# Kernel tuning notes

Hardware: AMD Instinct MI355X
Metric: run time of the kernel (lower is better)

The kernel has to match this reference:

```python
import jax, jax.numpy as jnp
import numpy as np

EPSILON = 0.0014  # ODIN perturbation magnitude (init kwarg)


def _penultimate(x, W, b):
    # Simple feature extractor standing in for model.penultimate_forward:
    # flatten image and apply ReLU(linear). feat: [B, D]
    B = x.shape[0]
    return jax.nn.relu(x.reshape(B, -1) @ W + b)


def _mahalanobis_scores(feat, mu, invsig):
    # diff: [B, C, D]; y[b,c] = -diff[b,c] @ invsig @ diff[b,c]
    # Fused as a single einsum instead of the naive [B,C,D,D] broadcast.
    diff = feat[:, None, :] - mu[None, :, :]
    return -jnp.einsum('bcd,de,bce->bc', diff, invsig, diff)


def setup_inputs() -> dict:
    key = jax.random.key(0)
    k1, k2, k3, k4, k5 = jax.random.split(key, 5)
    B, C, D, IN = 1024, 100, 512, 3 * 32 * 32
    x = jax.random.uniform(k1, (B, 3, 32, 32), dtype=jnp.float32)
    W = jax.random.normal(k2, (IN, D), dtype=jnp.float32) * (1.0 / np.sqrt(IN))
    b = jax.random.normal(k3, (D,), dtype=jnp.float32) * 0.01
    mu = jax.random.normal(k4, (C, D), dtype=jnp.float32)
    # symmetric positive-definite inverse covariance
    A = jax.random.normal(k5, (D, D), dtype=jnp.float32) * (1.0 / np.sqrt(D))
    invsig = A @ A.T + jnp.eye(D, dtype=jnp.float32)
    return {"x": x, "W": W, "b": b, "mu": mu, "invsig": invsig}


def reference(x, W, b, mu, invsig):
    # FGSM step: perturb x toward increasing the max class score.
    def fgsm_loss(xx):
        y = _mahalanobis_scores(_penultimate(xx, W, b), mu, invsig)
        return jnp.max(y, axis=1).sum()

    g = jax.grad(fgsm_loss)(x)
    # torch.autograd.grad(create_graph=False) detaches the grad -> stop_gradient
    x_adv = jnp.clip(x + EPSILON * jax.lax.stop_gradient(g), 0.0, 1.0)
    # Main pass on the perturbed input.
    return _mahalanobis_scores(_penultimate(x_adv, W, b), mu, invsig)
```

## Files before the change

### kernel.cpp

```cpp
#include <hip/hip_runtime.h>
#include <hip/hip_bf16.h>

#define EPS_ODIN 0.0014f

constexpr int Bb  = 1024;
constexpr int Cc  = 100;
constexpr int Dd  = 512;
constexpr int INn = 3072;
constexpr int PITCH = 68;

using s16x8 = __attribute__((ext_vector_type(8))) short;
using s16x4 = __attribute__((ext_vector_type(4))) short;
using f32x4 = __attribute__((ext_vector_type(4))) float;

__device__ __forceinline__ short f2bf(float f) {
    __hip_bfloat16 h = __float2bfloat16(f);
    return *reinterpret_cast<short*>(&h);
}

__global__ __launch_bounds__(256) void prep_kernel(
    const float* __restrict__ x, const float* __restrict__ W,
    const float* __restrict__ invsig, const float* __restrict__ mu,
    short* __restrict__ x_b, short* __restrict__ Wt_b,
    short* __restrict__ is_b, short* __restrict__ mu_b)
{
    __shared__ float tp[32][33];
    const int tid = threadIdx.x, bid = blockIdx.x;
    const long gstride = (long)gridDim.x * 256;
    auto cvt4 = [&](const float* in, short* ob, long q) {
        long idx = q * 4;
        f32x4 v = *(const f32x4*)(in + idx);
        s16x4 o;
        #pragma unroll
        for (int j = 0; j < 4; ++j) o[j] = f2bf(v[j]);
        *(s16x4*)(ob + idx) = o;
    };
    for (long i = (long)bid * 256 + tid; i < (long)Bb * INn / 4; i += gstride) cvt4(x, x_b, i);
    for (long i = (long)bid * 256 + tid; i < (long)Dd * Dd / 4; i += gstride) cvt4(invsig, is_b, i);
    for (long i = (long)bid * 256 + tid; i < (long)112 * Dd / 4; i += gstride) {
        long idx = i * 4;
        if ((idx >> 9) < Cc) cvt4(mu, mu_b, i);
        else *(s16x4*)(mu_b + idx) = s16x4{0, 0, 0, 0};
    }

    const int tx = tid & 31, ty = tid >> 5;
    for (int tix = bid; tix < (INn / 32) * (Dd / 32); tix += gridDim.x) {
        int r0 = (tix >> 4) * 32, c0 = (tix & 15) * 32;
        #pragma unroll
        for (int i2 = 0; i2 < 4; ++i2)
            tp[ty + i2 * 8][tx] = W[(long)(r0 + ty + i2 * 8) * Dd + c0 + tx];
        __syncthreads();
        #pragma unroll
        for (int i2 = 0; i2 < 4; ++i2) {
            int c = c0 + ty + i2 * 8;
            Wt_b[(long)c * INn + r0 + tx] = f2bf(tp[tx][ty + i2 * 8]);
        }
        __syncthreads();
    }
}

__global__ __launch_bounds__(256) void im_q_kernel(
    const float* __restrict__ mu, const float* __restrict__ invsig,
    float* __restrict__ im, float* __restrict__ q)
{
    __shared__ float muc[512];
    __shared__ float red[4];
    const int tid = threadIdx.x, c = blockIdx.x;
    for (int e = tid; e < 512; e += 256) muc[e] = mu[(long)c * 512 + e];
    __syncthreads();
    const int d0 = tid, d1 = tid + 256;
    float a0 = 0.f, a1 = 0.f, a2 = 0.f, a3 = 0.f;
    for (int e = 0; e < 512; e += 2) {
        float m0 = muc[e], m1 = muc[e + 1];
        a0 = fmaf(m0, invsig[(long)e * 512 + d0], a0);
        a1 = fmaf(m0, invsig[(long)e * 512 + d1], a1);
        a2 = fmaf(m1, invsig[(long)(e + 1) * 512 + d0], a2);
        a3 = fmaf(m1, invsig[(long)(e + 1) * 512 + d1], a3);
    }
    float r0 = a0 + a2, r1 = a1 + a3;
    im[(long)c * 512 + d0] = r0;
    im[(long)c * 512 + d1] = r1;
    float s = muc[d0] * r0 + muc[d1] * r1;
    #pragma unroll
    for (int off = 32; off; off >>= 1) s += __shfl_down(s, off);
    if ((tid & 63) == 0) red[tid >> 6] = s;
    __syncthreads();
    if (tid == 0) q[c] = red[0] + red[1] + red[2] + red[3];
}

template<int EPI>
__global__ __launch_bounds__(256, 4) void gemm_b1(
    const short* __restrict__ A, const short* __restrict__ Bm,
    float* __restrict__ Cm, long K, int kcount, int N, long sstr,
    const float* __restrict__ aux1, const float* __restrict__ aux2,
    short* __restrict__ obf, float esc)
{
    __shared__ short As[128 * PITCH];
    __shared__ short Bs[64 * PITCH];
    const int tid = threadIdx.x;
    const int m0 = blockIdx.y * 128, n0 = blockIdx.x * 64;
    const long kbeg = (long)blockIdx.z * kcount;
    const int lane = tid & 63, w = tid >> 6, wm = w * 32;
    const int lrow = lane & 15, kseg = lane >> 4;
    const int srow = tid >> 3, skc = (tid & 7) * 8;
    const int nkt = kcount >> 6;

    f32x4 acc[2][4];
    #pragma unroll
    for (int i = 0; i < 2; ++i)
        #pragma unroll
        for (int j = 0; j < 4; ++j)
            acc[i][j] = f32x4{0.f, 0.f, 0.f, 0.f};

    s16x8 rA[4], rB[2];
    auto ldA = [&](int kt) {
        #pragma unroll
        for (int i = 0; i < 4; ++i)
            rA[i] = *(const s16x8*)(A + (long)(m0 + srow + i * 32) * K + kbeg + (long)kt * 64 + skc);
    };
    auto ldB = [&](int kt) {
        #pragma unroll
        for (int i = 0; i < 2; ++i)
            rB[i] = *(const s16x8*)(Bm + (long)(n0 + srow + i * 32) * K + kbeg + (long)kt * 64 + skc);
    };

    ldA(0); ldB(0);
    for (int kt = 0; kt < nkt; ++kt) {
        #pragma unroll
        for (int i = 0; i < 4; ++i)
            *(s16x8*)&As[(srow + i * 32) * PITCH + skc] = rA[i];
        #pragma unroll
        for (int i = 0; i < 2; ++i)
            *(s16x8*)&Bs[(srow + i * 32) * PITCH + skc] = rB[i];
        __syncthreads();
        if (kt + 1 < nkt) { ldA(kt + 1); ldB(kt + 1); }
        #pragma unroll
        for (int kk = 0; kk < 2; ++kk) {
            s16x8 ah[2], bfr[4];
            #pragma unroll
            for (int i = 0; i < 2; ++i)
                ah[i] = *(const s16x8*)&As[(wm + i * 16 + lrow) * PITCH + kk * 32 + kseg * 8];
            #pragma unroll
            for (int j = 0; j < 4; ++j)
                bfr[j] = *(const s16x8*)&Bs[(j * 16 + lrow) * PITCH + kk * 32 + kseg * 8];
            #pragma unroll
            for (int i = 0; i < 2; ++i)
                #pragma unroll
                for (int j = 0; j < 4; ++j)
                    acc[i][j] = __builtin_amdgcn_mfma_f32_16x16x32_bf16(ah[i], bfr[j], acc[i][j], 0, 0, 0);
        }
        __syncthreads();
    }

    const int crow = (lane >> 4) * 4, ccol = lane & 15;
    #pragma unroll
    for (int i = 0; i < 2; ++i)
        #pragma unroll
        for (int j = 0; j < 4; ++j)
            #pragma unroll
            for (int r = 0; r < 4; ++r) {
                int gm = m0 + wm + i * 16 + crow + r;
                int gn = n0 + j * 16 + ccol;
                float v = acc[i][j][r];
                if (EPI == 0) {
                    (Cm + (long)blockIdx.z * sstr)[(long)gm * 512 + gn] = v;
                } else if (EPI == 1) {
                    long cidx = (long)gm * N + gn;
                    Cm[cidx] = v;
                    obf[cidx] = f2bf(v);
                } else {
                    long cidx = (long)gm * N + gn;
                    float u = fmaxf(aux1[cidx] + aux2[gn] + esc * v, 0.f);
                    Cm[cidx] = u;
                    obf[cidx] = f2bf(u);
                }
            }
}

__global__ __launch_bounds__(256) void reduce_feat(
    const float* __restrict__ part, const float* __restrict__ bias,
    float* __restrict__ featpre, float* __restrict__ feat, short* __restrict__ fb)
{
    long idx = ((long)blockIdx.x * 256 + threadIdx.x) * 4;
    f32x4 v = *(const f32x4*)(part + idx);
    #pragma unroll
    for (int z = 1; z < 4; ++z)
        v += *(const f32x4*)(part + (long)z * Bb * Dd + idx);
    *(f32x4*)(featpre + idx) = v;
    f32x4 bb = *(const f32x4*)(bias + (idx & 511));
    s16x4 o;
    #pragma unroll
    for (int j = 0; j < 4; ++j) {
        v[j] = fmaxf(v[j] + bb[j], 0.f);
        o[j] = f2bf(v[j]);
    }
    *(f32x4*)(feat + idx) = v;
    *(s16x4*)(fb + idx) = o;
}

__global__ __launch_bounds__(256) void reduce_wtw(
    const float* __restrict__ wpart, short* __restrict__ wtw_b)
{
    long idx = ((long)blockIdx.x * 256 + threadIdx.x) * 4;
    f32x4 v = *(const f32x4*)(wpart + idx);
    #pragma unroll
    for (int z = 1; z < 4; ++z)
        v += *(const f32x4*)(wpart + (long)z * Dd * Dd + idx);
    s16x4 o;
    #pragma unroll
    for (int j = 0; j < 4; ++j) o[j] = f2bf(v[j]);
    *(s16x4*)(wtw_b + idx) = o;
}

__global__ __launch_bounds__(256) void tail_a(
    const short* __restrict__ h_b, const short* __restrict__ mu_b,
    const float* __restrict__ feat, const float* __restrict__ hbuf,
    const float* __restrict__ im, const float* __restrict__ q,
    short* __restrict__ dz_b)
{
    __shared__ f32x4 red[4][7][64];
    __shared__ int cstv[16];
    const int tid = threadIdx.x, lane = tid & 63, w = tid >> 6;
    const int m0 = blockIdx.x * 16;
    const int arow = lane & 15, kseg = lane >> 4;

    f32x4 acc[7];
    #pragma unroll
    for (int j = 0; j < 7; ++j) acc[j] = f32x4{0.f, 0.f, 0.f, 0.f};

    const long abase = (long)(m0 + arow) * 512 + w * 128 + kseg * 8;
    const long bbase = (long)arow * 512 + w * 128 + kseg * 8;
    #pragma unroll
    for (int kt = 0; kt < 4; ++kt) {
        s16x8 av = *(const s16x8*)(h_b + abase + kt * 32);
        #pragma unroll
        for (int j = 0; j < 7; ++j) {
            s16x8 bv = *(const s16x8*)(mu_b + bbase + (long)j * 16 * 512 + kt * 32);
            acc[j] = __builtin_amdgcn_mfma_f32_16x16x32_bf16(av, bv, acc[j], 0, 0, 0);
        }
    }
    #pragma unroll
    for (int j = 0; j < 7; ++j) red[w][j][lane] = acc[j];
    __syncthreads();

    if (w == 0) {
        #pragma unroll
        for (int j = 0; j < 7; ++j) {
            f32x4 s0 = red[0][j][lane];
            #pragma unroll
            for (int ww = 1; ww < 4; ++ww) s0 += red[ww][j][lane];
            acc[j] = s0;
        }
        const int crow = (lane >> 4) * 4, ccol = lane & 15;
        #pragma unroll
        for (int r = 0; r < 4; ++r) {
            float best = -INFINITY; int bestc = 0;
            #pragma unroll
            for (int j = 0; j < 7; ++j) {
                int n = j * 16 + ccol;
                if (n < 100) {
                    float v = 2.f * acc[j][r] - q[n];
                    if (v > best) { best = v; bestc = n; }
                }
            }
            #pragma unroll
            for (int mk = 1; mk <= 8; mk <<= 1) {
                float ov = __shfl_xor(best, mk);
                int   oc = __shfl_xor(bestc, mk);
                if (ov > best || (ov == best && oc < bestc)) { best = ov; bestc = oc; }
            }
            if (ccol == 0) cstv[crow + r] = bestc;
        }
    }
    __syncthreads();

    #pragma unroll
    for (int it = 0; it < 8; ++it) {
        int i4 = it * 256 + tid;
        int r = i4 >> 7, d4 = (i4 & 127) * 4;
        long gi = (long)(m0 + r) * 512 + d4;
        f32x4 fv = *(const f32x4*)(feat + gi);
        f32x4 hv = *(const f32x4*)(hbuf + gi);
        f32x4 iv = *(const f32x4*)(im + (long)cstv[r] * 512 + d4);
        s16x4 o;
        #pragma unroll
        for (int jj = 0; jj < 4; ++jj) {
            float v = (fv[jj] > 0.f) ? -2.f * (hv[jj] - iv[jj]) : 0.f;
            o[jj] = f2bf(v);
        }
        *(s16x4*)(dz_b + gi) = o;
    }
}

__global__ __launch_bounds__(256) void tail_b(
    const short* __restrict__ h_b, const short* __restrict__ mu_b,
    const float* __restrict__ feat, const float* __restrict__ hbuf,
    const float* __restrict__ q, float* __restrict__ out)
{
    __shared__ f32x4 red[4][7][64];
    __shared__ float srow[16];
    const int tid = threadIdx.x, lane = tid & 63, w = tid >> 6;
    const int m0 = blockIdx.x * 16;
    const int arow = lane & 15, kseg = lane >> 4;

    #pragma unroll
    for (int rr = 0; rr < 4; ++rr) {
        int r = w * 4 + rr;
        long gi = (long)(m0 + r) * 512 + lane * 8;
        f32x4 a0 = *(const f32x4*)(feat + gi);
        f32x4 a1 = *(const f32x4*)(feat + gi + 4);
        f32x4 b0 = *(const f32x4*)(hbuf + gi);
        f32x4 b1 = *(const f32x4*)(hbuf + gi + 4);
        float ss = 0.f;
        #pragma unroll
        for (int jj = 0; jj < 4; ++jj) ss += a0[jj] * b0[jj] + a1[jj] * b1[jj];
        #pragma unroll
        for (int off = 32; off; off >>= 1) ss += __shfl_down(ss, off);
        if (lane == 0) srow[r] = ss;
    }

    f32x4 acc[7];
    #pragma unroll
    for (int j = 0; j < 7; ++j) acc[j] = f32x4{0.f, 0.f, 0.f, 0.f};
    const long abase = (long)(m0 + arow) * 512 + w * 128 + kseg * 8;
    const long bbase = (long)arow * 512 + w * 128 + kseg * 8;
    #pragma unroll
    for (int kt = 0; kt < 4; ++kt) {
        s16x8 av = *(const s16x8*)(h_b + abase + kt * 32);
        #pragma unroll
        for (int j = 0; j < 7; ++j) {
            s16x8 bv = *(const s16x8*)(mu_b + bbase + (long)j * 16 * 512 + kt * 32);
            acc[j] = __builtin_amdgcn_mfma_f32_16x16x32_bf16(av, bv, acc[j], 0, 0, 0);
        }
    }
    #pragma unroll
    for (int j = 0; j < 7; ++j) red[w][j][lane] = acc[j];
    __syncthreads();

    if (w == 0) {
        const int crow = (lane >> 4) * 4, ccol = lane & 15;
        #pragma unroll
        for (int j = 0; j < 7; ++j) {
            int n = j * 16 + ccol;
            if (n >= 100) continue;
            f32x4 s0 = red[0][j][lane];
            #pragma unroll
            for (int ww = 1; ww < 4; ++ww) s0 += red[ww][j][lane];
            float qn = q[n];
            #pragma unroll
            for (int r = 0; r < 4; ++r)
                out[(long)(m0 + crow + r) * 100 + n] = 2.f * s0[r] - srow[crow + r] - qn;
        }
    }
}

extern "C" void kernel_launch(void* const* d_in, const int* in_sizes, int n_in,
                              void* d_out, int out_size, void* d_ws, size_t ws_size,
                              hipStream_t stream)
{
    const float* x      = (const float*)d_in[0];
    const float* W      = (const float*)d_in[1];
    const float* bias   = (const float*)d_in[2];
    const float* mu     = (const float*)d_in[3];
    const float* invsig = (const float*)d_in[4];
    float* out = (float*)d_out;

    char* wp = (char*)d_ws;
    auto alloc = [&](size_t bytes) { char* p = wp; wp += (bytes + 255) & ~size_t(255); return p; };
    short* x_b   = (short*)alloc((size_t)Bb * INn * 2);
    short* Wt_b  = (short*)alloc((size_t)Dd * INn * 2);
    short* is_b  = (short*)alloc((size_t)Dd * Dd * 2);
    short* mu_b  = (short*)alloc((size_t)112 * Dd * 2);
    short* wtw_b = (short*)alloc((size_t)Dd * Dd * 2);
    float* im    = (float*)alloc((size_t)Cc * Dd * 4);
    float* q     = (float*)alloc(512);
    float* part  = (float*)alloc((size_t)4 * Bb * Dd * 4);
    float* wpart = (float*)alloc((size_t)4 * Dd * Dd * 4);
    float* featpre = (float*)alloc((size_t)Bb * Dd * 4);
    float* feat  = (float*)alloc((size_t)Bb * Dd * 4);
    short* f_b   = (short*)alloc((size_t)Bb * Dd * 2);
    float* hbuf  = (float*)alloc((size_t)Bb * Dd * 4);
    short* h_b   = (short*)alloc((size_t)Bb * Dd * 2);
    short* dz_b  = (short*)alloc((size_t)Bb * Dd * 2);

    dim3 blk(256);

    prep_kernel<<<512, blk, 0, stream>>>(x, W, invsig, mu, x_b, Wt_b, is_b, mu_b);
    im_q_kernel<<<Cc, blk, 0, stream>>>(mu, invsig, im, q);
    gemm_b1<0><<<dim3(8, 4, 4), blk, 0, stream>>>(
        Wt_b, Wt_b, wpart, INn, INn / 4, Dd, (long)Dd * Dd, nullptr, nullptr, nullptr, 0.f);
    reduce_wtw<<<256, blk, 0, stream>>>(wpart, wtw_b);
    gemm_b1<0><<<dim3(8, 8, 4), blk, 0, stream>>>(
        x_b, Wt_b, part, INn, INn / 4, Dd, (long)Bb * Dd, nullptr, nullptr, nullptr, 0.f);
    reduce_feat<<<512, blk, 0, stream>>>(part, bias, featpre, feat, f_b);
    gemm_b1<1><<<dim3(8, 8), blk, 0, stream>>>(
        f_b, is_b, hbuf, Dd, Dd, Dd, 0, nullptr, nullptr, h_b, 0.f);
    tail_a<<<Bb / 16, blk, 0, stream>>>(h_b, mu_b, feat, hbuf, im, q, dz_b);
    gemm_b1<3><<<dim3(8, 8), blk, 0, stream>>>(
        dz_b, wtw_b, feat, Dd, Dd, Dd, 0, featpre, bias, f_b, EPS_ODIN);
    gemm_b1<1><<<dim3(8, 8), blk, 0, stream>>>(
        f_b, is_b, hbuf, Dd, Dd, Dd, 0, nullptr, nullptr, h_b, 0.f);
    tail_b<<<Bb / 16, blk, 0, stream>>>(h_b, mu_b, feat, hbuf, q, out);
}
```

Baseline: 109.2 us.

## Fold mu·invsig rows into invsig GEMM to compute class scores directly

Appends the precomputed rows invsig·mu_c (in bf16) under invsig, so a single GEMM of features against this 640-row matrix yields both h = f·invsig and f·invsig·mu_c. The tail kernels then no longer run a second MFMA product of h against mu, and they shrink to 4 rows per block with simple argmax and score assembly. This removes the bf16 rounding of h before the class dot product and the h_b buffer, at the cost of an extra column tile in the GEMM and a different rounding path (mu folded through invsig in fp32 and then rounded).

Result: faster. 99.99 us (median of 2 runs) (-8.5%).

```diff
diff --git a/kernel.cpp b/kernel.cpp
--- a/kernel.cpp
+++ b/kernel.cpp
@@ -20,9 +20,8 @@
 
 __global__ __launch_bounds__(256) void prep_kernel(
     const float* __restrict__ x, const float* __restrict__ W,
-    const float* __restrict__ invsig, const float* __restrict__ mu,
-    short* __restrict__ x_b, short* __restrict__ Wt_b,
-    short* __restrict__ is_b, short* __restrict__ mu_b)
+    const float* __restrict__ invsig,
+    short* __restrict__ x_b, short* __restrict__ Wt_b, short* __restrict__ ism_b)
 {
     __shared__ float tp[32][33];
     const int tid = threadIdx.x, bid = blockIdx.x;
@@ -36,12 +35,9 @@
         *(s16x4*)(ob + idx) = o;
     };
     for (long i = (long)bid * 256 + tid; i < (long)Bb * INn / 4; i += gstride) cvt4(x, x_b, i);
-    for (long i = (long)bid * 256 + tid; i < (long)Dd * Dd / 4; i += gstride) cvt4(invsig, is_b, i);
-    for (long i = (long)bid * 256 + tid; i < (long)112 * Dd / 4; i += gstride) {
-        long idx = i * 4;
-        if ((idx >> 9) < Cc) cvt4(mu, mu_b, i);
-        else *(s16x4*)(mu_b + idx) = s16x4{0, 0, 0, 0};
-    }
+    for (long i = (long)bid * 256 + tid; i < (long)Dd * Dd / 4; i += gstride) cvt4(invsig, ism_b, i);
+    for (long i = (long)bid * 256 + tid; i < 28 * 512 / 4; i += gstride)
+        *(s16x4*)(ism_b + (long)612 * 512 + i * 4) = s16x4{0, 0, 0, 0};
 
     const int tx = tid & 31, ty = tid >> 5;
     for (int tix = bid; tix < (INn / 32) * (Dd / 32); tix += gridDim.x) {
@@ -61,7 +57,7 @@
 
 __global__ __launch_bounds__(256) void im_q_kernel(
     const float* __restrict__ mu, const float* __restrict__ invsig,
-    float* __restrict__ im, float* __restrict__ q)
+    float* __restrict__ im, float* __restrict__ q, short* __restrict__ ism_b)
 {
     __shared__ float muc[512];
     __shared__ float red[4];
@@ -80,6 +76,8 @@
     float r0 = a0 + a2, r1 = a1 + a3;
     im[(long)c * 512 + d0] = r0;
     im[(long)c * 512 + d1] = r1;
+    ism_b[(long)(512 + c) * 512 + d0] = f2bf(r0);
+    ism_b[(long)(512 + c) * 512 + d1] = f2bf(r1);
     float s = muc[d0] * r0 + muc[d1] * r1;
     #pragma unroll
     for (int off = 32; off; off >>= 1) s += __shfl_down(s, off);
@@ -164,10 +162,6 @@
                 float v = acc[i][j][r];
                 if (EPI == 0) {
                     (Cm + (long)blockIdx.z * sstr)[(long)gm * 512 + gn] = v;
-                } else if (EPI == 1) {
-                    long cidx = (long)gm * N + gn;
-                    Cm[cidx] = v;
-                    obf[cidx] = f2bf(v);
                 } else {
                     long cidx = (long)gm * N + gn;
                     float u = fmaxf(aux1[cidx] + aux2[gn] + esc * v, 0.f);
@@ -177,6 +171,85 @@
             }
 }
 
+__global__ __launch_bounds__(256, 4) void gemm_ht(
+    const short* __restrict__ A, const short* __restrict__ Bm,
+    float* __restrict__ hbuf, float* __restrict__ tbuf)
+{
+    __shared__ short As[128 * PITCH];
+    __shared__ short Bs[64 * PITCH];
+    const int tid = threadIdx.x;
+    const int m0 = blockIdx.y * 128, n0 = blockIdx.x * 64;
+    const int lane = tid & 63, w = tid >> 6, wm = w * 32;
+    const int lrow = lane & 15, kseg = lane >> 4;
+    const int srow = tid >> 3, skc = (tid & 7) * 8;
+
+    f32x4 acc[2][4];
+    #pragma unroll
+    for (int i = 0; i < 2; ++i)
+        #pragma unroll
+        for (int j = 0; j < 4; ++j)
+            acc[i][j] = f32x4{0.f, 0.f, 0.f, 0.f};
+
+    s16x8 rA[4], rB[2];
+    auto ldA = [&](int kt) {
+        #pragma unroll
+        for (int i = 0; i < 4; ++i)
+            rA[i] = *(const s16x8*)(A + (long)(m0 + srow + i * 32) * 512 + kt * 64 + skc);
+    };
+    auto ldB = [&](int kt) {
+        #pragma unroll
+        for (int i = 0; i < 2; ++i)
+            rB[i] = *(const s16x8*)(Bm + (long)(n0 + srow + i * 32) * 512 + kt * 64 + skc);
+    };
+
+    ldA(0); ldB(0);
+    for (int kt = 0; kt < 8; ++kt) {
+        #pragma unroll
+        for (int i = 0; i < 4; ++i)
+            *(s16x8*)&As[(srow + i * 32) * PITCH + skc] = rA[i];
+        #pragma unroll
+        for (int i = 0; i < 2; ++i)
+            *(s16x8*)&Bs[(srow + i * 32) * PITCH + skc] = rB[i];
+        __syncthreads();
+        if (kt + 1 < 8) { ldA(kt + 1); ldB(kt + 1); }
+        #pragma unroll
+        for (int kk = 0; kk < 2; ++kk) {
+            s16x8 ah[2], bfr[4];
+            #pragma unroll
+            for (int i = 0; i < 2; ++i)
+                ah[i] = *(const s16x8*)&As[(wm + i * 16 + lrow) * PITCH + kk * 32 + kseg * 8];
+            #pragma unroll
+            for (int j = 0; j < 4; ++j)
+                bfr[j] = *(const s16x8*)&Bs[(j * 16 + lrow) * PITCH + kk * 32 + kseg * 8];
+            #pragma unroll
+            for (int i = 0; i < 2; ++i)
+                #pragma unroll
+                for (int j = 0; j < 4; ++j)
+                    acc[i][j] = __builtin_amdgcn_mfma_f32_16x16x32_bf16(ah[i], bfr[j], acc[i][j], 0, 0, 0);
+        }
+        __syncthreads();
+    }
+
+    const int crow = (lane >> 4) * 4, ccol = lane & 15;
+    if (n0 < 512) {
+        #pragma unroll
+        for (int i = 0; i < 2; ++i)
+            #pragma unroll
+            for (int j = 0; j < 4; ++j)
+                #pragma unroll
+                for (int r = 0; r < 4; ++r)
+                    hbuf[(long)(m0 + wm + i * 16 + crow + r) * 512 + n0 + j * 16 + ccol] = acc[i][j][r];
+    } else {
+        #pragma unroll
+        for (int i = 0; i < 2; ++i)
+            #pragma unroll
+            for (int j = 0; j < 4; ++j)
+                #pragma unroll
+                for (int r = 0; r < 4; ++r)
+                    tbuf[(long)(m0 + wm + i * 16 + crow + r) * 128 + (n0 - 512) + j * 16 + ccol] = acc[i][j][r];
+    }
+}
+
 __global__ __launch_bounds__(256) void reduce_feat(
     const float* __restrict__ part, const float* __restrict__ bias,
     float* __restrict__ featpre, float* __restrict__ feat, short* __restrict__ fb)
@@ -212,70 +285,35 @@
     *(s16x4*)(wtw_b + idx) = o;
 }
 
-__global__ __launch_bounds__(256) void tail_a(
-    const short* __restrict__ h_b, const short* __restrict__ mu_b,
+__global__ __launch_bounds__(256) void tail_a2(
+    const float* __restrict__ tbuf, const float* __restrict__ q,
     const float* __restrict__ feat, const float* __restrict__ hbuf,
-    const float* __restrict__ im, const float* __restrict__ q,
-    short* __restrict__ dz_b)
-{
-    __shared__ f32x4 red[4][7][64];
-    __shared__ int cstv[16];
+    const float* __restrict__ im, short* __restrict__ dz_b)
+{
+    __shared__ int cstv[4];
     const int tid = threadIdx.x, lane = tid & 63, w = tid >> 6;
-    const int m0 = blockIdx.x * 16;
-    const int arow = lane & 15, kseg = lane >> 4;
-
-    f32x4 acc[7];
-    #pragma unroll
-    for (int j = 0; j < 7; ++j) acc[j] = f32x4{0.f, 0.f, 0.f, 0.f};
-
-    const long abase = (long)(m0 + arow) * 512 + w * 128 + kseg * 8;
-    const long bbase = (long)arow * 512 + w * 128 + kseg * 8;
-    #pragma unroll
-    for (int kt = 0; kt < 4; ++kt) {
-        s16x8 av = *(const s16x8*)(h_b + abase + kt * 32);
-        #pragma unroll
-        for (int j = 0; j < 7; ++j) {
-            s16x8 bv = *(const s16x8*)(mu_b + bbase + (long)j * 16 * 512 + kt * 32);
-            acc[j] = __builtin_amdgcn_mfma_f32_16x16x32_bf16(av, bv, acc[j], 0, 0, 0);
-        }
-    }
-    #pragma unroll
-    for (int j = 0; j < 7; ++j) red[w][j][lane] = acc[j];
+    const int m0 = blockIdx.x * 4;
+
+    {
+        const float* tr = tbuf + (long)(m0 + w) * 128;
+        float best = 2.f * tr[lane] - q[lane];
+        int bestc = lane;
+        if (lane + 64 < 100) {
+            float v1 = 2.f * tr[lane + 64] - q[lane + 64];
+            if (v1 > best) { best = v1; bestc = lane + 64; }
+        }
+        #pragma unroll
+        for (int mk = 1; mk <= 32; mk <<= 1) {
+            float ov = __shfl_xor(best, mk);
+            int   oc = __shfl_xor(bestc, mk);
+            if (ov > best || (ov == best && oc < bestc)) { best = ov; bestc = oc; }
+        }
+        if (lane == 0) cstv[w] = bestc;
+    }
     __syncthreads();
 
-    if (w == 0) {
-        #pragma unroll
-        for (int j = 0; j < 7; ++j) {
-            f32x4 s0 = red[0][j][lane];
-            #pragma unroll
-            for (int ww = 1; ww < 4; ++ww) s0 += red[ww][j][lane];
-            acc[j] = s0;
-        }
-        const int crow = (lane >> 4) * 4, ccol = lane & 15;
-        #pragma unroll
-        for (int r = 0; r < 4; ++r) {
-            float best = -INFINITY; int bestc = 0;
-            #pragma unroll
-            for (int j = 0; j < 7; ++j) {
-                int n = j * 16 + ccol;
-                if (n < 100) {
-                    float v = 2.f * acc[j][r] - q[n];
-                    if (v > best) { best = v; bestc = n; }
-                }
-            }
-            #pragma unroll
-            for (int mk = 1; mk <= 8; mk <<= 1) {
-                float ov = __shfl_xor(best, mk);
-                int   oc = __shfl_xor(bestc, mk);
-                if (ov > best || (ov == best && oc < bestc)) { best = ov; bestc = oc; }
-            }
-            if (ccol == 0) cstv[crow + r] = bestc;
-        }
-    }
-    __syncthreads();
-
-    #pragma unroll
-    for (int it = 0; it < 8; ++it) {
+    #pragma unroll
+    for (int it = 0; it < 2; ++it) {
         int i4 = it * 256 + tid;
         int r = i4 >> 7, d4 = (i4 & 127) * 4;
         long gi = (long)(m0 + r) * 512 + d4;
@@ -292,21 +330,17 @@
     }
 }
 
-__global__ __launch_bounds__(256) void tail_b(
-    const short* __restrict__ h_b, const short* __restrict__ mu_b,
+__global__ __launch_bounds__(256) void tail_b2(
+    const float* __restrict__ tbuf, const float* __restrict__ q,
     const float* __restrict__ feat, const float* __restrict__ hbuf,
-    const float* __restrict__ q, float* __restrict__ out)
-{
-    __shared__ f32x4 red[4][7][64];
-    __shared__ float srow[16];
+    float* __restrict__ out)
+{
+    __shared__ float srow[4];
     const int tid = threadIdx.x, lane = tid & 63, w = tid >> 6;
-    const int m0 = blockIdx.x * 16;
-    const int arow = lane & 15, kseg = lane >> 4;
-
-    #pragma unroll
-    for (int rr = 0; rr < 4; ++rr) {
-        int r = w * 4 + rr;
-        long gi = (long)(m0 + r) * 512 + lane * 8;
+    const int m0 = blockIdx.x * 4;
+
+    {
+        long gi = (long)(m0 + w) * 512 + lane * 8;
         f32x4 a0 = *(const f32x4*)(feat + gi);
         f32x4 a1 = *(const f32x4*)(feat + gi + 4);
         f32x4 b0 = *(const f32x4*)(hbuf + gi);
@@ -316,40 +350,16 @@
         for (int jj = 0; jj < 4; ++jj) ss += a0[jj] * b0[jj] + a1[jj] * b1[jj];
         #pragma unroll
         for (int off = 32; off; off >>= 1) ss += __shfl_down(ss, off);
-        if (lane == 0) srow[r] = ss;
-    }
-
-    f32x4 acc[7];
-    #pragma unroll
-    for (int j = 0; j < 7; ++j) acc[j] = f32x4{0.f, 0.f, 0.f, 0.f};
-    const long abase = (long)(m0 + arow) * 512 + w * 128 + kseg * 8;
-    const long bbase = (long)arow * 512 + w * 128 + kseg * 8;
-    #pragma unroll
-    for (int kt = 0; kt < 4; ++kt) {
-        s16x8 av = *(const s16x8*)(h_b + abase + kt * 32);
-        #pragma unroll
-        for (int j = 0; j < 7; ++j) {
-            s16x8 bv = *(const s16x8*)(mu_b + bbase + (long)j * 16 * 512 + kt * 32);
-            acc[j] = __builtin_amdgcn_mfma_f32_16x16x32_bf16(av, bv, acc[j], 0, 0, 0);
-        }
-    }
-    #pragma unroll
-    for (int j = 0; j < 7; ++j) red[w][j][lane] = acc[j];
+        if (lane == 0) srow[w] = ss;
+    }
     __syncthreads();
 
-    if (w == 0) {
-        const int crow = (lane >> 4) * 4, ccol = lane & 15;
-        #pragma unroll
-        for (int j = 0; j < 7; ++j) {
-            int n = j * 16 + ccol;
-            if (n >= 100) continue;
-            f32x4 s0 = red[0][j][lane];
-            #pragma unroll
-            for (int ww = 1; ww < 4; ++ww) s0 += red[ww][j][lane];
-            float qn = q[n];
-            #pragma unroll
-            for (int r = 0; r < 4; ++r)
-                out[(long)(m0 + crow + r) * 100 + n] = 2.f * s0[r] - srow[crow + r] - qn;
+    #pragma unroll
+    for (int it = 0; it < 2; ++it) {
+        int i = it * 256 + tid;
+        if (i < 400) {
+            int r = i / 100, c = i - r * 100;
+            out[(long)(m0 + r) * 100 + c] = 2.f * tbuf[(long)(m0 + r) * 128 + c] - srow[r] - q[c];
         }
     }
 }
@@ -369,8 +379,7 @@
     auto alloc = [&](size_t bytes) { char* p = wp; wp += (bytes + 255) & ~size_t(255); return p; };
     short* x_b   = (short*)alloc((size_t)Bb * INn * 2);
     short* Wt_b  = (short*)alloc((size_t)Dd * INn * 2);
-    short* is_b  = (short*)alloc((size_t)Dd * Dd * 2);
-    short* mu_b  = (short*)alloc((size_t)112 * Dd * 2);
+    short* ism_b = (short*)alloc((size_t)640 * Dd * 2);
     short* wtw_b = (short*)alloc((size_t)Dd * Dd * 2);
     float* im    = (float*)alloc((size_t)Cc * Dd * 4);
     float* q     = (float*)alloc(512);
@@ -380,25 +389,23 @@
     float* feat  = (float*)alloc((size_t)Bb * Dd * 4);
     short* f_b   = (short*)alloc((size_t)Bb * Dd * 2);
     float* hbuf  = (float*)alloc((size_t)Bb * Dd * 4);
-    short* h_b   = (short*)alloc((size_t)Bb * Dd * 2);
+    float* tbuf  = (float*)alloc((size_t)Bb * 128 * 4);
     short* dz_b  = (short*)alloc((size_t)Bb * Dd * 2);
 
     dim3 blk(256);
 
-    prep_kernel<<<512, blk, 0, stream>>>(x, W, invsig, mu, x_b, Wt_b, is_b, mu_b);
-    im_q_kernel<<<Cc, blk, 0, stream>>>(mu, invsig, im, q);
+    prep_kernel<<<512, blk, 0, stream>>>(x, W, invsig, x_b, Wt_b, ism_b);
+    im_q_kernel<<<Cc, blk, 0, stream>>>(mu, invsig, im, q, ism_b);
     gemm_b1<0><<<dim3(8, 4, 4), blk, 0, stream>>>(
         Wt_b, Wt_b, wpart, INn, INn / 4, Dd, (long)Dd * Dd, nullptr, nullptr, nullptr, 0.f);
     reduce_wtw<<<256, blk, 0, stream>>>(wpart, wtw_b);
     gemm_b1<0><<<dim3(8, 8, 4), blk, 0, stream>>>(
         x_b, Wt_b, part, INn, INn / 4, Dd, (long)Bb * Dd, nullptr, nullptr, nullptr, 0.f);
     reduce_feat<<<512, blk, 0, stream>>>(part, bias, featpre, feat, f_b);
-    gemm_b1<1><<<dim3(8, 8), blk, 0, stream>>>(
-        f_b, is_b, hbuf, Dd, Dd, Dd, 0, nullptr, nullptr, h_b, 0.f);
-    tail_a<<<Bb / 16, blk, 0, stream>>>(h_b, mu_b, feat, hbuf, im, q, dz_b);
+    gemm_ht<<<dim3(10, 8), blk, 0, stream>>>(f_b, ism_b, hbuf, tbuf);
+    tail_a2<<<Bb / 4, blk, 0, stream>>>(tbuf, q, feat, hbuf, im, dz_b);
     gemm_b1<3><<<dim3(8, 8), blk, 0, stream>>>(
         dz_b, wtw_b, feat, Dd, Dd, Dd, 0, featpre, bias, f_b, EPS_ODIN);
-    gemm_b1<1><<<dim3(8, 8), blk, 0, stream>>>(
-        f_b, is_b, hbuf, Dd, Dd, Dd, 0, nullptr, nullptr, h_b, 0.f);
-    tail_b<<<Bb / 16, blk, 0, stream>>>(h_b, mu_b, feat, hbuf, q, out);
-}
+    gemm_ht<<<dim3(10, 8), blk, 0, stream>>>(f_b, ism_b, hbuf, tbuf);
+    tail_b2<<<Bb / 4, blk, 0, stream>>>(tbuf, q, feat, hbuf, out);
+}
```
